# Kernel tuning notes

Measured on AMD Instinct MI355X. Metric: run time of the kernel, lower is better.

Reference implementation:

```python
import jax, jax.numpy as jnp
import numpy as np

B, T, I, H, L = 32, 1024, 512, 1024, 2
SPARSITY = 0.1
SPECTRAL_RADIUS = 0.9


def _make_reservoir(seed, h):
    rng = np.random.default_rng(seed)
    W = rng.normal(size=(h, h)).astype(np.float32)
    mask = rng.random((h, h)) < SPARSITY
    W = W * mask
    rho = np.max(np.abs(np.linalg.eigvals(W)))
    return jnp.asarray(W * (SPECTRAL_RADIUS / rho), dtype=jnp.float32)


def _dense(rng_seed, shape, fan_in):
    rng = np.random.default_rng(rng_seed)
    return jnp.asarray(rng.normal(size=shape).astype(np.float32) / np.sqrt(fan_in))


def setup_inputs() -> dict:
    key = jax.random.key(0)
    k_x = jax.random.fold_in(key, 1)
    x = jax.random.normal(k_x, (B, T, I), dtype=jnp.float32)
    h0 = jnp.zeros((L, B, H), dtype=jnp.float32)
    # layer 0: input_size -> hidden_size
    W_in0 = _dense(10, (H, I), I)
    W_res0 = _make_reservoir(11, H)
    W_z0 = _dense(12, (H, I), I)
    U_z0 = _dense(13, (H, H), H)
    b_z0 = jnp.zeros((H,), dtype=jnp.float32)
    # layer 1: hidden_size -> hidden_size
    W_in1 = _dense(20, (H, H), H)
    W_res1 = _make_reservoir(21, H)
    W_z1 = _dense(22, (H, H), H)
    U_z1 = _dense(23, (H, H), H)
    b_z1 = jnp.zeros((H,), dtype=jnp.float32)
    return dict(x=x, h0=h0,
                W_in0=W_in0, W_res0=W_res0, W_z0=W_z0, U_z0=U_z0, b_z0=b_z0,
                W_in1=W_in1, W_res1=W_res1, W_z1=W_z1, U_z1=U_z1, b_z1=b_z1)


def _cell(x_t, h, W_in, W_res, W_z, U_z, b_z):
    # GRU-style gated echo-state cell
    z = jax.nn.sigmoid(x_t @ W_z.T + h @ U_z.T + b_z)
    h_tilde = jnp.tanh(x_t @ W_in.T + h @ W_res.T)
    return (1.0 - z) * h + z * h_tilde


def reference(x, h0, W_in0, W_res0, W_z0, U_z0, b_z0,
              W_in1, W_res1, W_z1, U_z1, b_z1):
    xT = jnp.transpose(x, (1, 0, 2))  # (T, B, I) since batch_first=True

    def step(carry, x_t):
        h_l0, h_l1 = carry
        h_l0 = _cell(x_t, h_l0, W_in0, W_res0, W_z0, U_z0, b_z0)
        h_l1 = _cell(h_l0, h_l1, W_in1, W_res1, W_z1, U_z1, b_z1)
        return (h_l0, h_l1), h_l1

    (hf0, hf1), outs = jax.lax.scan(step, (h0[0], h0[1]), xT)
    output = jnp.transpose(outs, (1, 0, 2))  # (B, T, H)
    h_n = jnp.stack([hf0, hf1], axis=0)      # (L, B, H)
    return output, h_n
```

## Files before the change

kernel.cpp:

```cpp
#include <hip/hip_runtime.h>


#define T_STEPS 1024

typedef __attribute__((ext_vector_type(8))) short  bf16x8;
typedef __attribute__((ext_vector_type(4))) float  floatx4;

static __device__ __forceinline__ unsigned short f2bf(float f) {
  union { float f; unsigned u; } c; c.f = f;
  unsigned r = c.u + 0x7FFFu + ((c.u >> 16) & 1u);
  return (unsigned short)(r >> 16);
}
static __device__ __forceinline__ float bf2f(unsigned short s) {
  union { unsigned u; float f; } c; c.u = ((unsigned)s) << 16; return c.f;
}

static __device__ __forceinline__ void llc_load4(const void* p, floatx4& r) {
  asm volatile("global_load_dwordx4 %0, %1, off sc0 sc1" : "=v"(r) : "v"(p));
}
static __device__ __forceinline__ void llc_store_short(unsigned short* p, unsigned v) {
  asm volatile("global_store_short %0, %1, off sc0 sc1" :: "v"(p), "v"(v) : "memory");
}
static __device__ __forceinline__ void flush_vm() {
  asm volatile("s_waitcnt vmcnt(0)" ::: "memory");
}
#define WAITQ8(N, q) asm volatile("s_waitcnt vmcnt(" #N ")" \
  : "+v"((q)[0]), "+v"((q)[1]), "+v"((q)[2]), "+v"((q)[3]), \
    "+v"((q)[4]), "+v"((q)[5]), "+v"((q)[6]), "+v"((q)[7]) :: "memory")

static __device__ __forceinline__ void poll16(const int* row, int lane) {
  const int* a = row + (lane & 15);
  for (;;) {
    int v = __hip_atomic_load(a, __ATOMIC_RELAXED, __HIP_MEMORY_SCOPE_AGENT);
    if (__all(v != 0)) break;
    __builtin_amdgcn_s_sleep(1);
  }
  asm volatile("" ::: "memory");
}
static __device__ __forceinline__ void poll_ge(const int* row, int lane, int target) {
  for (;;) {
    int v = __hip_atomic_load(row + lane, __ATOMIC_RELAXED, __HIP_MEMORY_SCOPE_AGENT);
    if (__all(v >= target)) break;
    __builtin_amdgcn_s_sleep(1);
  }
  asm volatile("" ::: "memory");
}

__global__ __launch_bounds__(512, 2) void esgp_v3(
    const float* __restrict__ x,
    const float* __restrict__ W_in0, const float* __restrict__ W_res0,
    const float* __restrict__ W_z0,  const float* __restrict__ U_z0,
    const float* __restrict__ b_z0,
    const float* __restrict__ W_in1, const float* __restrict__ W_res1,
    const float* __restrict__ W_z1,  const float* __restrict__ U_z1,
    const float* __restrict__ b_z1,
    float* __restrict__ dout,
    int* f0, int* f1, int* prog1,
    unsigned short* r0h, unsigned short* r0l,
    unsigned short* r1h, unsigned short* r1l)
{
  __shared__ float s_part[8][2][2][256];
  __shared__ float s_hprev[512];
  __shared__ float s_bias[16];

  const int tid  = threadIdx.x, lane = tid & 63, wid = tid >> 6;
  const int quad = lane >> 4, m = lane & 15;
  const int layer = blockIdx.x >> 6, jb = blockIdx.x & 63;
  const int jbase = jb * 16, jrow = jbase + m;

  s_hprev[tid] = 0.f;
  if (tid < 16) s_bias[tid] = (layer ? b_z1 : b_z0)[jbase + tid];

  unsigned short* oH = layer ? r1h : r0h;
  unsigned short* oL = layer ? r1l : r0l;

  auto loadW = [&](const float* W, int Kfull, int kofs, int nkt,
                   bf16x8* whi, bf16x8* wlo) {
    const float* wr = W + (size_t)jrow * Kfull + kofs + quad * 8;
    for (int kt = 0; kt < nkt; ++kt) {
      floatx4 v0 = *(const floatx4*)(wr + kt * 32);
      floatx4 v1 = *(const floatx4*)(wr + kt * 32 + 4);
      bf16x8 h, l;
      #pragma unroll
      for (int e = 0; e < 8; ++e) {
        float f = (e < 4) ? v0[e] : v1[e - 4];
        unsigned short hb = f2bf(f);
        h[e] = (short)hb;
        l[e] = (short)f2bf(f - bf2f(hb));
      }
      whi[kt] = h; wlo[kt] = l;
    }
  };

  auto gate = [&](int t) {
    const int b = wid * 4 + quad, bt = b >> 4;
    const int fi = (b & 15) * 16 + m;
    float zp = s_bias[m], tp2 = 0.f;
    #pragma unroll
    for (int w = 0; w < 8; ++w) {
      zp  += s_part[w][0][bt][fi];
      tp2 += s_part[w][1][bt][fi];
    }
    float sg = 1.f / (1.f + __expf(-zp));
    float th = 1.f - 2.f / (__expf(2.f * tp2) + 1.f);
    float hp = s_hprev[tid];
    float hn = hp + sg * (th - hp);
    s_hprev[tid] = hn;
    unsigned short hb = f2bf(hn);
    unsigned short lb = f2bf(hn - bf2f(hb));
    const int ri = (t & 7) * 32768 + b * 1024 + jbase + m;
    llc_store_short(oH + ri, (unsigned)hb);
    llc_store_short(oL + ri, (unsigned)lb);
    if (layer) dout[((size_t)b * T_STEPS + t) * 1024 + jbase + m] = hn;
    if (t == T_STEPS - 1)
      dout[(size_t)33554432 + (size_t)layer * 32768 + (size_t)b * 1024 + jbase + m] = hn;
    flush_vm();
    __syncthreads();
    if (tid == 0) {
      if (layer) {
        __hip_atomic_store(f1 + t * 64 + jb, 1, __ATOMIC_RELAXED, __HIP_MEMORY_SCOPE_AGENT);
        __hip_atomic_store(prog1 + jb, t + 1, __ATOMIC_RELAXED, __HIP_MEMORY_SCOPE_AGENT);
      } else {
        __hip_atomic_store(f0 + t * 64 + jb, 1, __ATOMIC_RELAXED, __HIP_MEMORY_SCOPE_AGENT);
      }
    }
  };

  if (layer == 1 || wid < 4) {
    const float* Wz; const float* Wt;
    const unsigned short* pAh; const unsigned short* pAl;
    const int* fArr; int tOff;
    if (layer == 0)      { Wz = U_z0; Wt = W_res0; pAh = r0h; pAl = r0l; fArr = f0; tOff = 1; }
    else if (wid < 4)    { Wz = W_z1; Wt = W_in1;  pAh = r0h; pAl = r0l; fArr = f0; tOff = 0; }
    else                 { Wz = U_z1; Wt = W_res1; pAh = r1h; pAl = r1l; fArr = f1; tOff = 1; }
    const int wsub = wid & 3, kslice = wsub * 256;

    bf16x8 wzh[8], wzl[8], wth[8], wtl[8];
    loadW(Wz, 1024, kslice, 8, wzh, wzl);
    loadW(Wt, 1024, kslice, 8, wth, wtl);
    __syncthreads();

    for (int t = 0; t < T_STEPS; ++t) {
      const int tp = t - tOff;
      if (tp >= 0) poll16(fArr + tp * 64 + wsub * 16, lane);
      if (layer == 0 && t >= 8 && (t & 3) == 0) poll_ge(prog1, lane, t - 4);

      const int slot = tp & 7;
      const unsigned short* bh = pAh + slot * 32768;
      const unsigned short* bl = pAl + slot * 32768;

      floatx4 q0[8], q1[8];
      floatx4 accz[2] = {{0,0,0,0},{0,0,0,0}};
      floatx4 acct[2] = {{0,0,0,0},{0,0,0,0}};

      auto issueG = [&](int g, floatx4* Q) {
        const int kb = kslice + g * 64 + quad * 8;
        #pragma unroll
        for (int kt2 = 0; kt2 < 2; ++kt2)
          #pragma unroll
          for (int bt = 0; bt < 2; ++bt) {
            const int off = (bt * 16 + m) * 1024 + kb + kt2 * 32;
            llc_load4(bh + off, Q[(kt2 * 2 + bt) * 2 + 0]);
            llc_load4(bl + off, Q[(kt2 * 2 + bt) * 2 + 1]);
          }
      };
      auto mfmaG = [&](int g, floatx4* Q) {
        #pragma unroll
        for (int kt2 = 0; kt2 < 2; ++kt2) {
          const int kg = g * 2 + kt2;
          #pragma unroll
          for (int bt = 0; bt < 2; ++bt) {
            bf16x8 ah = *(bf16x8*)&Q[(kt2 * 2 + bt) * 2 + 0];
            bf16x8 al = *(bf16x8*)&Q[(kt2 * 2 + bt) * 2 + 1];
            accz[bt] = __builtin_amdgcn_mfma_f32_16x16x32_bf16(ah, wzh[kg], accz[bt], 0, 0, 0);
            accz[bt] = __builtin_amdgcn_mfma_f32_16x16x32_bf16(al, wzh[kg], accz[bt], 0, 0, 0);
            accz[bt] = __builtin_amdgcn_mfma_f32_16x16x32_bf16(ah, wzl[kg], accz[bt], 0, 0, 0);
            acct[bt] = __builtin_amdgcn_mfma_f32_16x16x32_bf16(ah, wth[kg], acct[bt], 0, 0, 0);
            acct[bt] = __builtin_amdgcn_mfma_f32_16x16x32_bf16(al, wth[kg], acct[bt], 0, 0, 0);
            acct[bt] = __builtin_amdgcn_mfma_f32_16x16x32_bf16(ah, wtl[kg], acct[bt], 0, 0, 0);
          }
        }
      };

      issueG(0, q0); issueG(1, q1);
      WAITQ8(8, q0); mfmaG(0, q0); issueG(2, q0);
      WAITQ8(8, q1); mfmaG(1, q1); issueG(3, q1);
      WAITQ8(8, q0); mfmaG(2, q0);
      WAITQ8(0, q1); mfmaG(3, q1);

      #pragma unroll
      for (int r = 0; r < 4; ++r) {
        #pragma unroll
        for (int bt = 0; bt < 2; ++bt) {
          s_part[wid][0][bt][(quad * 4 + r) * 16 + m] = accz[bt][r];
          s_part[wid][1][bt][(quad * 4 + r) * 16 + m] = acct[bt][r];
        }
      }
      __syncthreads();
      gate(t);
    }
  } else {
    const int wsub2 = wid - 4, kofs = wsub2 * 128;
    bf16x8 wzh[4], wzl[4], wth[4], wtl[4];
    loadW(W_z0,  512, kofs, 4, wzh, wzl);
    loadW(W_in0, 512, kofs, 4, wth, wtl);
    __syncthreads();

    for (int t = 0; t < T_STEPS; ++t) {
      if (t >= 8 && (t & 3) == 0) poll_ge(prog1, lane, t - 4);

      floatx4 xa[16];
      const float* xb = x + (size_t)t * 512 + kofs + quad * 8;
      #pragma unroll
      for (int kt = 0; kt < 4; ++kt)
        #pragma unroll
        for (int bt = 0; bt < 2; ++bt) {
          const float* p = xb + (size_t)(bt * 16 + m) * 524288 + kt * 32;
          xa[(kt * 2 + bt) * 2 + 0] = *(const floatx4*)p;
          xa[(kt * 2 + bt) * 2 + 1] = *(const floatx4*)(p + 4);
        }

      floatx4 accz[2] = {{0,0,0,0},{0,0,0,0}};
      floatx4 acct[2] = {{0,0,0,0},{0,0,0,0}};
      #pragma unroll
      for (int kt = 0; kt < 4; ++kt)
        #pragma unroll
        for (int bt = 0; bt < 2; ++bt) {
          floatx4 v0 = xa[(kt * 2 + bt) * 2 + 0];
          floatx4 v1 = xa[(kt * 2 + bt) * 2 + 1];
          bf16x8 ah, al;
          #pragma unroll
          for (int e = 0; e < 8; ++e) {
            float f = (e < 4) ? v0[e] : v1[e - 4];
            unsigned short hb = f2bf(f);
            ah[e] = (short)hb;
            al[e] = (short)f2bf(f - bf2f(hb));
          }
          accz[bt] = __builtin_amdgcn_mfma_f32_16x16x32_bf16(ah, wzh[kt], accz[bt], 0, 0, 0);
          accz[bt] = __builtin_amdgcn_mfma_f32_16x16x32_bf16(al, wzh[kt], accz[bt], 0, 0, 0);
          accz[bt] = __builtin_amdgcn_mfma_f32_16x16x32_bf16(ah, wzl[kt], accz[bt], 0, 0, 0);
          acct[bt] = __builtin_amdgcn_mfma_f32_16x16x32_bf16(ah, wth[kt], acct[bt], 0, 0, 0);
          acct[bt] = __builtin_amdgcn_mfma_f32_16x16x32_bf16(al, wth[kt], acct[bt], 0, 0, 0);
          acct[bt] = __builtin_amdgcn_mfma_f32_16x16x32_bf16(ah, wtl[kt], acct[bt], 0, 0, 0);
        }

      #pragma unroll
      for (int r = 0; r < 4; ++r) {
        #pragma unroll
        for (int bt = 0; bt < 2; ++bt) {
          s_part[wid][0][bt][(quad * 4 + r) * 16 + m] = accz[bt][r];
          s_part[wid][1][bt][(quad * 4 + r) * 16 + m] = acct[bt][r];
        }
      }
      __syncthreads();
      gate(t);
    }
  }
}

extern "C" void kernel_launch(void* const* d_in, const int* in_sizes, int n_in,
                              void* d_out, int out_size, void* d_ws, size_t ws_size,
                              hipStream_t stream) {
  const float* x      = (const float*)d_in[0];
  const float* W_in0  = (const float*)d_in[2];
  const float* W_res0 = (const float*)d_in[3];
  const float* W_z0   = (const float*)d_in[4];
  const float* U_z0   = (const float*)d_in[5];
  const float* b_z0   = (const float*)d_in[6];
  const float* W_in1  = (const float*)d_in[7];
  const float* W_res1 = (const float*)d_in[8];
  const float* W_z1   = (const float*)d_in[9];
  const float* U_z1   = (const float*)d_in[10];
  const float* b_z1   = (const float*)d_in[11];
  float* out = (float*)d_out;

  char* ws = (char*)d_ws;
  int*   f0    = (int*)(ws + 0x000000);
  int*   f1    = (int*)(ws + 0x040000);
  int*   prog1 = (int*)(ws + 0x080000);
  unsigned short* r0h = (unsigned short*)(ws + 0x100000);
  unsigned short* r0l = (unsigned short*)(ws + 0x180000);
  unsigned short* r1h = (unsigned short*)(ws + 0x200000);
  unsigned short* r1l = (unsigned short*)(ws + 0x280000);

  hipMemsetAsync(d_ws, 0, 0x300000, stream);

  esgp_v3<<<dim3(128), dim3(512), 0, stream>>>(
      x, W_in0, W_res0, W_z0, U_z0, b_z0,
      W_in1, W_res1, W_z1, U_z1, b_z1,
      out, f0, f1, prog1, r0h, r0l, r1h, r1l);
}
```

Measured before the change: 10.56 ms.

## Replace per-block flag publish with per-wave atomic counters and double-buffered partials

Each wave now atomically increments a per-step counter once its own stores have drained, replacing the block-wide barrier plus single-thread flag store. Consumers poll until the counter reaches 8 using pipelined loads whose results are tied into the first vmcnt wait. The partial-sum shared buffer is double-buffered by step parity so the trailing barrier can be dropped. The layer-1 progress counter is now published before the gate. This cuts one barrier and some flag latency from the serial critical path per timestep, at the cost of more atomic traffic and subtler ordering between waves.

New measurement: 16.75 ms. 1.59x slower.

```diff
diff --git a/kernel.cpp b/kernel.cpp
--- a/kernel.cpp
+++ b/kernel.cpp
@@ -27,16 +27,11 @@
 #define WAITQ8(N, q) asm volatile("s_waitcnt vmcnt(" #N ")" \
   : "+v"((q)[0]), "+v"((q)[1]), "+v"((q)[2]), "+v"((q)[3]), \
     "+v"((q)[4]), "+v"((q)[5]), "+v"((q)[6]), "+v"((q)[7]) :: "memory")
-
-static __device__ __forceinline__ void poll16(const int* row, int lane) {
-  const int* a = row + (lane & 15);
-  for (;;) {
-    int v = __hip_atomic_load(a, __ATOMIC_RELAXED, __HIP_MEMORY_SCOPE_AGENT);
-    if (__all(v != 0)) break;
-    __builtin_amdgcn_s_sleep(1);
-  }
-  asm volatile("" ::: "memory");
-}
+#define WAITQ8F(N, q, a, b) asm volatile("s_waitcnt vmcnt(" #N ")" \
+  : "+v"((q)[0]), "+v"((q)[1]), "+v"((q)[2]), "+v"((q)[3]), \
+    "+v"((q)[4]), "+v"((q)[5]), "+v"((q)[6]), "+v"((q)[7]), \
+    "+v"(a), "+v"(b) :: "memory")
+
 static __device__ __forceinline__ void poll_ge(const int* row, int lane, int target) {
   for (;;) {
     int v = __hip_atomic_load(row + lane, __ATOMIC_RELAXED, __HIP_MEMORY_SCOPE_AGENT);
@@ -46,7 +41,7 @@
   asm volatile("" ::: "memory");
 }
 
-__global__ __launch_bounds__(512, 2) void esgp_v3(
+__global__ __launch_bounds__(512, 2) void esgp_v4(
     const float* __restrict__ x,
     const float* __restrict__ W_in0, const float* __restrict__ W_res0,
     const float* __restrict__ W_z0,  const float* __restrict__ U_z0,
@@ -59,7 +54,7 @@
     unsigned short* r0h, unsigned short* r0l,
     unsigned short* r1h, unsigned short* r1l)
 {
-  __shared__ float s_part[8][2][2][256];
+  __shared__ float s_part[2][8][2][2][256];
   __shared__ float s_hprev[512];
   __shared__ float s_bias[16];
 
@@ -73,6 +68,7 @@
 
   unsigned short* oH = layer ? r1h : r0h;
   unsigned short* oL = layer ? r1l : r0l;
+  int* fRow = layer ? f1 : f0;
 
   auto loadW = [&](const float* W, int Kfull, int kofs, int nkt,
                    bf16x8* whi, bf16x8* wlo) {
@@ -93,13 +89,14 @@
   };
 
   auto gate = [&](int t) {
+    const int p = t & 1;
     const int b = wid * 4 + quad, bt = b >> 4;
     const int fi = (b & 15) * 16 + m;
     float zp = s_bias[m], tp2 = 0.f;
     #pragma unroll
     for (int w = 0; w < 8; ++w) {
-      zp  += s_part[w][0][bt][fi];
-      tp2 += s_part[w][1][bt][fi];
+      zp  += s_part[p][w][0][bt][fi];
+      tp2 += s_part[p][w][1][bt][fi];
     }
     float sg = 1.f / (1.f + __expf(-zp));
     float th = 1.f - 2.f / (__expf(2.f * tp2) + 1.f);
@@ -111,19 +108,13 @@
     const int ri = (t & 7) * 32768 + b * 1024 + jbase + m;
     llc_store_short(oH + ri, (unsigned)hb);
     llc_store_short(oL + ri, (unsigned)lb);
+    flush_vm();
+    if (lane == 0)
+      __hip_atomic_fetch_add(fRow + t * 64 + jb, 1,
+                             __ATOMIC_RELAXED, __HIP_MEMORY_SCOPE_AGENT);
     if (layer) dout[((size_t)b * T_STEPS + t) * 1024 + jbase + m] = hn;
     if (t == T_STEPS - 1)
       dout[(size_t)33554432 + (size_t)layer * 32768 + (size_t)b * 1024 + jbase + m] = hn;
-    flush_vm();
-    __syncthreads();
-    if (tid == 0) {
-      if (layer) {
-        __hip_atomic_store(f1 + t * 64 + jb, 1, __ATOMIC_RELAXED, __HIP_MEMORY_SCOPE_AGENT);
-        __hip_atomic_store(prog1 + jb, t + 1, __ATOMIC_RELAXED, __HIP_MEMORY_SCOPE_AGENT);
-      } else {
-        __hip_atomic_store(f0 + t * 64 + jb, 1, __ATOMIC_RELAXED, __HIP_MEMORY_SCOPE_AGENT);
-      }
-    }
   };
 
   if (layer == 1 || wid < 4) {
@@ -140,10 +131,25 @@
     loadW(Wt, 1024, kslice, 8, wth, wtl);
     __syncthreads();
 
+    int pv0 = 8, pv1 = 8;
+
+    auto pollc = [&](const int* row) {
+      const int* a = row + (lane & 15);
+      asm volatile("global_load_dword %0, %1, off sc0 sc1" : "=v"(pv0) : "v"(a));
+      for (;;) {
+        asm volatile("global_load_dword %0, %1, off sc0 sc1" : "=v"(pv1) : "v"(a));
+        asm volatile("s_waitcnt vmcnt(1)" : "+v"(pv0) :: "memory");
+        if (__all(pv0 >= 8)) break;
+        asm volatile("global_load_dword %0, %1, off sc0 sc1" : "=v"(pv0) : "v"(a));
+        asm volatile("s_waitcnt vmcnt(1)" : "+v"(pv1) :: "memory");
+        if (__all(pv1 >= 8)) break;
+      }
+    };
+
     for (int t = 0; t < T_STEPS; ++t) {
+      if (layer == 0 && t >= 8 && (t & 3) == 0) poll_ge(prog1, lane, t - 4);
       const int tp = t - tOff;
-      if (tp >= 0) poll16(fArr + tp * 64 + wsub * 16, lane);
-      if (layer == 0 && t >= 8 && (t & 3) == 0) poll_ge(prog1, lane, t - 4);
+      if (tp >= 0) pollc(fArr + tp * 64 + wsub * 16);
 
       const int slot = tp & 7;
       const unsigned short* bh = pAh + slot * 32768;
@@ -183,7 +189,8 @@
       };
 
       issueG(0, q0); issueG(1, q1);
-      WAITQ8(8, q0); mfmaG(0, q0); issueG(2, q0);
+      WAITQ8F(8, q0, pv0, pv1);
+      mfmaG(0, q0); issueG(2, q0);
       WAITQ8(8, q1); mfmaG(1, q1); issueG(3, q1);
       WAITQ8(8, q0); mfmaG(2, q0);
       WAITQ8(0, q1); mfmaG(3, q1);
@@ -192,11 +199,13 @@
       for (int r = 0; r < 4; ++r) {
         #pragma unroll
         for (int bt = 0; bt < 2; ++bt) {
-          s_part[wid][0][bt][(quad * 4 + r) * 16 + m] = accz[bt][r];
-          s_part[wid][1][bt][(quad * 4 + r) * 16 + m] = acct[bt][r];
+          s_part[t & 1][wid][0][bt][(quad * 4 + r) * 16 + m] = accz[bt][r];
+          s_part[t & 1][wid][1][bt][(quad * 4 + r) * 16 + m] = acct[bt][r];
         }
       }
       __syncthreads();
+      if (layer && tid == 0)
+        __hip_atomic_store(prog1 + jb, t + 1, __ATOMIC_RELAXED, __HIP_MEMORY_SCOPE_AGENT);
       gate(t);
     }
   } else {
@@ -248,8 +257,8 @@
       for (int r = 0; r < 4; ++r) {
         #pragma unroll
         for (int bt = 0; bt < 2; ++bt) {
-          s_part[wid][0][bt][(quad * 4 + r) * 16 + m] = accz[bt][r];
-          s_part[wid][1][bt][(quad * 4 + r) * 16 + m] = acct[bt][r];
+          s_part[t & 1][wid][0][bt][(quad * 4 + r) * 16 + m] = accz[bt][r];
+          s_part[t & 1][wid][1][bt][(quad * 4 + r) * 16 + m] = acct[bt][r];
         }
       }
       __syncthreads();
@@ -285,7 +294,7 @@
 
   hipMemsetAsync(d_ws, 0, 0x300000, stream);
 
-  esgp_v3<<<dim3(128), dim3(512), 0, stream>>>(
+  esgp_v4<<<dim3(128), dim3(512), 0, stream>>>(
       x, W_in0, W_res0, W_z0, U_z0, b_z0,
       W_in1, W_res1, W_z1, U_z1, b_z1,
       out, f0, f1, prog1, r0h, r0l, r1h, r1l);
```

## Tag hidden-state bf16 LSB with epoch bit and validate cached loads with retry

Applied to the files above, without the earlier changes.

Stores a generation tag in the lowest mantissa bit of each bf16 hi/lo hidden-state value, so readers can tell whether data is current. The main loads now go through the normal cache path instead of bypassing to the last-level cache, and each group is checked for the expected tag. Any mismatched group is reloaded with the bypassing loads until it matches. This aims to cut the latency of coherent loads, at the cost of one mantissa bit of precision in both halves plus validation ALU work and possible retry loops. The flag polling is still kept, so the synchronization is partly redundant.

Measured after the change: 14.46 ms. 1.37x slower.

```diff
diff --git a/kernel.cpp b/kernel.cpp
--- a/kernel.cpp
+++ b/kernel.cpp
@@ -5,6 +5,7 @@
 
 typedef __attribute__((ext_vector_type(8))) short  bf16x8;
 typedef __attribute__((ext_vector_type(4))) float  floatx4;
+typedef __attribute__((ext_vector_type(4))) int    intx4;
 
 static __device__ __forceinline__ unsigned short f2bf(float f) {
   union { float f; unsigned u; } c; c.f = f;
@@ -17,6 +18,9 @@
 
 static __device__ __forceinline__ void llc_load4(const void* p, floatx4& r) {
   asm volatile("global_load_dwordx4 %0, %1, off sc0 sc1" : "=v"(r) : "v"(p));
+}
+static __device__ __forceinline__ void l2_load4(const void* p, floatx4& r) {
+  asm volatile("global_load_dwordx4 %0, %1, off" : "=v"(r) : "v"(p));
 }
 static __device__ __forceinline__ void llc_store_short(unsigned short* p, unsigned v) {
   asm volatile("global_store_short %0, %1, off sc0 sc1" :: "v"(p), "v"(v) : "memory");
@@ -46,7 +50,7 @@
   asm volatile("" ::: "memory");
 }
 
-__global__ __launch_bounds__(512, 2) void esgp_v3(
+__global__ __launch_bounds__(512, 2) void esgp_v6(
     const float* __restrict__ x,
     const float* __restrict__ W_in0, const float* __restrict__ W_res0,
     const float* __restrict__ W_z0,  const float* __restrict__ U_z0,
@@ -106,11 +110,14 @@
     float hp = s_hprev[tid];
     float hn = hp + sg * (th - hp);
     s_hprev[tid] = hn;
-    unsigned short hb = f2bf(hn);
-    unsigned short lb = f2bf(hn - bf2f(hb));
+    const unsigned tagbit = ((unsigned)((t >> 3) & 1)) ^ 1u;
+    unsigned hb = f2bf(hn);
+    hb = (hb & 0xFFFEu) | tagbit;
+    unsigned lb = f2bf(hn - bf2f((unsigned short)hb));
+    lb = (lb & 0xFFFEu) | tagbit;
     const int ri = (t & 7) * 32768 + b * 1024 + jbase + m;
-    llc_store_short(oH + ri, (unsigned)hb);
-    llc_store_short(oL + ri, (unsigned)lb);
+    llc_store_short(oH + ri, hb);
+    llc_store_short(oL + ri, lb);
     if (layer) dout[((size_t)b * T_STEPS + t) * 1024 + jbase + m] = hn;
     if (t == T_STEPS - 1)
       dout[(size_t)33554432 + (size_t)layer * 32768 + (size_t)b * 1024 + jbase + m] = hn;
@@ -148,12 +155,25 @@
       const int slot = tp & 7;
       const unsigned short* bh = pAh + slot * 32768;
       const unsigned short* bl = pAl + slot * 32768;
+      const unsigned want = (tp >= 0 && ((((tp >> 3) & 1) ^ 1) != 0)) ? 0x00010001u : 0u;
+      const bool doVal = (tp >= 0);
 
       floatx4 q0[8], q1[8];
       floatx4 accz[2] = {{0,0,0,0},{0,0,0,0}};
       floatx4 acct[2] = {{0,0,0,0},{0,0,0,0}};
 
       auto issueG = [&](int g, floatx4* Q) {
+        const int kb = kslice + g * 64 + quad * 8;
+        #pragma unroll
+        for (int kt2 = 0; kt2 < 2; ++kt2)
+          #pragma unroll
+          for (int bt = 0; bt < 2; ++bt) {
+            const int off = (bt * 16 + m) * 1024 + kb + kt2 * 32;
+            l2_load4(bh + off, Q[(kt2 * 2 + bt) * 2 + 0]);
+            l2_load4(bl + off, Q[(kt2 * 2 + bt) * 2 + 1]);
+          }
+      };
+      auto issueB = [&](int g, floatx4* Q) {
         const int kb = kslice + g * 64 + quad * 8;
         #pragma unroll
         for (int kt2 = 0; kt2 < 2; ++kt2)
@@ -163,6 +183,21 @@
             llc_load4(bh + off, Q[(kt2 * 2 + bt) * 2 + 0]);
             llc_load4(bl + off, Q[(kt2 * 2 + bt) * 2 + 1]);
           }
+      };
+      auto valRetry = [&](int g, floatx4* Q) {
+        if (!doVal) return;
+        for (;;) {
+          unsigned bad = 0;
+          #pragma unroll
+          for (int i = 0; i < 8; ++i) {
+            const intx4 w = *(const intx4*)&Q[i];
+            bad |= (unsigned)((w[0] ^ (int)want) | (w[1] ^ (int)want) |
+                              (w[2] ^ (int)want) | (w[3] ^ (int)want));
+          }
+          if (__all((bad & 0x00010001u) == 0u)) break;
+          issueB(g, Q);
+          WAITQ8(0, Q);
+        }
       };
       auto mfmaG = [&](int g, floatx4* Q) {
         #pragma unroll
@@ -183,10 +218,10 @@
       };
 
       issueG(0, q0); issueG(1, q1);
-      WAITQ8(8, q0); mfmaG(0, q0); issueG(2, q0);
-      WAITQ8(8, q1); mfmaG(1, q1); issueG(3, q1);
-      WAITQ8(8, q0); mfmaG(2, q0);
-      WAITQ8(0, q1); mfmaG(3, q1);
+      WAITQ8(8, q0); valRetry(0, q0); mfmaG(0, q0); issueG(2, q0);
+      WAITQ8(8, q1); valRetry(1, q1); mfmaG(1, q1); issueG(3, q1);
+      WAITQ8(8, q0); valRetry(2, q0); mfmaG(2, q0);
+      WAITQ8(0, q1); valRetry(3, q1); mfmaG(3, q1);
 
       #pragma unroll
       for (int r = 0; r < 4; ++r) {
@@ -285,7 +320,7 @@
 
   hipMemsetAsync(d_ws, 0, 0x300000, stream);
 
-  esgp_v3<<<dim3(128), dim3(512), 0, stream>>>(
+  esgp_v6<<<dim3(128), dim3(512), 0, stream>>>(
       x, W_in0, W_res0, W_z0, U_z0, b_z0,
       W_in1, W_res1, W_z1, U_z1, b_z1,
       out, f0, f1, prog1, r0h, r0l, r1h, r1l);
```
